# Kernel tuning notes

Hardware: AMD Instinct MI355X
Metric: run time of the kernel (lower is better)

The kernel has to match this reference:

```python
import jax, jax.numpy as jnp
import numpy as np

B, S, H, NH = 2, 2048, 1024, 16
D = H // NH

def setup_inputs() -> dict:
    key = jax.random.key(0)
    ks = jax.random.split(key, 9)
    s = 1.0 / np.sqrt(H)
    return {
        "x": jax.random.normal(ks[0], (B, S, H), jnp.float32),
        "wq": jax.random.uniform(ks[1], (H, H), jnp.float32, -s, s),
        "bq": jax.random.uniform(ks[2], (H,), jnp.float32, -s, s),
        "wk": jax.random.uniform(ks[3], (H, H), jnp.float32, -s, s),
        "bk": jax.random.uniform(ks[4], (H,), jnp.float32, -s, s),
        "wv": jax.random.uniform(ks[5], (H, H), jnp.float32, -s, s),
        "bv": jax.random.uniform(ks[6], (H,), jnp.float32, -s, s),
        "wo": jax.random.uniform(ks[7], (H, H), jnp.float32, -s, s),
        "bo": jax.random.uniform(ks[8], (H,), jnp.float32, -s, s),
    }

def _split_heads(t):
    # [B, S, H] -> [B, NH, S, D]
    return t.reshape(B, S, NH, D).transpose(0, 2, 1, 3)

def reference(x, wq, bq, wk, bk, wv, bv, wo, bo):
    q = _split_heads(x @ wq.T + bq)
    k = _split_heads(x @ wk.T + bk)
    v = _split_heads(x @ wv.T + bv)
    scores = jnp.einsum('bhqd,bhkd->bhqk', q, k) / jnp.sqrt(jnp.float32(D))
    attn = jax.nn.softmax(scores, axis=-1)  # full [B,NH,S,S] materialized as in source
    ctx = jnp.einsum('bhqk,bhkd->bhqd', attn, v)
    concat = ctx.transpose(0, 2, 1, 3).reshape(B, S, H)
    return concat @ wo.T + bo
```

## Files before the change

### kernel.cpp

```cpp
#include <hip/hip_runtime.h>
#include <cstdint>

typedef unsigned short u16;
typedef __attribute__((ext_vector_type(8))) short short8;
typedef __attribute__((ext_vector_type(4))) float f32x4;

#if __has_builtin(__builtin_amdgcn_exp2f)
#define EXP2F(x) __builtin_amdgcn_exp2f(x)
#else
#define EXP2F(x) exp2f(x)
#endif

__device__ inline u16 f2bf(float f) {
  union { float f; unsigned u; } v; v.f = f;
  unsigned u = v.u;
  return (u16)((u + 0x7fffu + ((u >> 16) & 1u)) >> 16);
}

__device__ inline unsigned pk2bf_fast(float a, float b) {
  union { float f; unsigned u; } ua, ub; ua.f = a; ub.f = b;
  return __builtin_amdgcn_perm(ub.u + 0x8000u, ua.u + 0x8000u, 0x07060302u);
}

__device__ inline void gl2lds16(const void* g, void* l) {
  __builtin_amdgcn_global_load_lds(
      (const __attribute__((address_space(1))) unsigned int*)(unsigned long long)(uintptr_t)g,
      (__attribute__((address_space(3))) unsigned int*)(unsigned int)(uintptr_t)l,
      16, 0, 0);
}


__global__ __launch_bounds__(256) void cvt_kernel(
    const float* __restrict__ x,
    const float* __restrict__ wq, const float* __restrict__ wk,
    const float* __restrict__ wv, const float* __restrict__ wo,
    u16* __restrict__ xb, u16* __restrict__ wqb, u16* __restrict__ wkb,
    u16* __restrict__ wvb, u16* __restrict__ wob) {
  const int y = blockIdx.y;
  const int Q = 1 << 20;
  const float* src;
  u16* dst;
  if (y < 4)       { src = x + y * Q; dst = xb + y * Q; }
  else if (y == 4) { src = wq; dst = wqb; }
  else if (y == 5) { src = wk; dst = wkb; }
  else if (y == 6) { src = wv; dst = wvb; }
  else             { src = wo; dst = wob; }
  const int i = (blockIdx.x * 256 + threadIdx.x) * 8;
  float4 a = *(const float4*)(src + i);
  float4 b = *(const float4*)(src + i + 4);
  short8 o;
  o[0] = (short)f2bf(a.x); o[1] = (short)f2bf(a.y);
  o[2] = (short)f2bf(a.z); o[3] = (short)f2bf(a.w);
  o[4] = (short)f2bf(b.x); o[5] = (short)f2bf(b.y);
  o[6] = (short)f2bf(b.z); o[7] = (short)f2bf(b.w);
  const int j = (i & ~63) | (((((i >> 3) & 7) ^ ((i >> 10) & 7))) << 3);
  *(short8*)(dst + j) = o;
}

__global__ __launch_bounds__(256) void gemm_qkv(
    const u16* __restrict__ xb,
    const u16* __restrict__ wqb, const u16* __restrict__ wkb, const u16* __restrict__ wvb,
    const float* __restrict__ bq, const float* __restrict__ bk, const float* __restrict__ bv,
    u16* __restrict__ qo, u16* __restrict__ ko, u16* __restrict__ vto) {
  const int z = blockIdx.z;
  const u16* W = (z == 0) ? wqb : (z == 1) ? wkb : wvb;
  const float* bias = (z == 0) ? bq : (z == 1) ? bk : bv;

  __shared__ u16 smem[32768];
  u16* As = smem;
  u16* Bs = smem + 16384;
  const int tid = threadIdx.x, lane = tid & 63;
  const int wid = tid >> 6, wm = wid >> 1, wn = wid & 1;
  const int l15 = lane & 15, lg = lane >> 4;
  const int m0 = blockIdx.y * 128, n0 = blockIdx.x * 128;
  const int sw = ((l15 & 7) << 3);

  f32x4 acc[4][4] = {};

#pragma unroll
  for (int i = 0; i < 4; ++i) {
    int c = i * 256 + tid;
    gl2lds16(xb + (m0 + (c >> 3)) * 1024 + (c & 7) * 8, As + c * 8);
    gl2lds16(W  + (n0 + (c >> 3)) * 1024 + (c & 7) * 8, Bs + c * 8);
  }

  for (int k0 = 0; k0 < 1024; k0 += 64) {
    const int p = (k0 >> 6) & 1;
    __syncthreads();
    if (k0 < 960) {
      u16* An = As + (1 - p) * 8192;
      u16* Bn = Bs + (1 - p) * 8192;
#pragma unroll
      for (int i = 0; i < 4; ++i) {
        int c = i * 256 + tid;
        gl2lds16(xb + (m0 + (c >> 3)) * 1024 + k0 + 64 + (c & 7) * 8, An + c * 8);
        gl2lds16(W  + (n0 + (c >> 3)) * 1024 + k0 + 64 + (c & 7) * 8, Bn + c * 8);
      }
    }
    const u16* Ap = As + p * 8192;
    const u16* Bp = Bs + p * 8192;
#pragma unroll
    for (int kk = 0; kk < 2; ++kk) {
      short8 af[4], bf[4];
#pragma unroll
      for (int mb = 0; mb < 4; ++mb)
        af[mb] = *(const short8*)(Ap + (wm * 64 + mb * 16 + l15) * 64 + ((((kk * 4 + lg) << 3) ^ sw)));
#pragma unroll
      for (int nb = 0; nb < 4; ++nb)
        bf[nb] = *(const short8*)(Bp + (wn * 64 + nb * 16 + l15) * 64 + ((((kk * 4 + lg) << 3) ^ sw)));
#pragma unroll
      for (int mb = 0; mb < 4; ++mb)
#pragma unroll
        for (int nb = 0; nb < 4; ++nb)
          acc[mb][nb] = __builtin_amdgcn_mfma_f32_16x16x32_bf16(af[mb], bf[nb], acc[mb][nb], 0, 0, 0);
    }
  }

  if (z < 2) {
    u16* out = (z == 0) ? qo : ko;
#pragma unroll
    for (int mb = 0; mb < 4; ++mb)
#pragma unroll
      for (int nb = 0; nb < 4; ++nb)
#pragma unroll
        for (int r = 0; r < 4; ++r) {
          int m = m0 + wm * 64 + mb * 16 + lg * 4 + r;
          int n = n0 + wn * 64 + nb * 16 + l15;
          float v = acc[mb][nb][r] + bias[n];
          int b = m >> 11, s = m & 2047, hh = n >> 6, d = n & 63;
          int dcol = (z == 0) ? d : ((((d >> 3) ^ (s & 7)) << 3) | (d & 7));
          out[((b * 16 + hh) * 2048 + s) * 64 + dcol] = f2bf(v);
        }
  } else {
    __syncthreads();
    u16* wbuf = smem + wid * 4608;
#pragma unroll
    for (int mb = 0; mb < 4; ++mb)
#pragma unroll
      for (int nb = 0; nb < 4; ++nb) {
        int n = n0 + wn * 64 + nb * 16 + l15;
        float bn = bias[n];
        int dl = nb * 16 + l15;
#pragma unroll
        for (int r = 0; r < 4; ++r) {
          int sig = (lg * 4 + r) * 4 + mb;
          wbuf[dl * 72 + sig] = f2bf(acc[mb][nb][r] + bn);
        }
      }
    int h_w = (n0 >> 6) + wn;
    int mbase = m0 + wm * 64;
    int b = mbase >> 11, sb = mbase & 2047;
#pragma unroll
    for (int i = 0; i < 8; ++i) {
      int dl = (lane >> 3) + 8 * i;
      int c = lane & 7;
      short8 vv = *(const short8*)(wbuf + dl * 72 + c * 8);
      int cs = c ^ (dl & 7);
      *(short8*)(vto + ((b * 16 + h_w) * 64 + dl) * 2048 + sb + cs * 8) = vv;
    }
  }
}

__global__ __launch_bounds__(256, 2) void attn_kernel(
    const u16* __restrict__ qg, const u16* __restrict__ kg,
    const u16* __restrict__ vtg, u16* __restrict__ ctxg) {
  const int h = blockIdx.x, qt = blockIdx.y, b = blockIdx.z;
  const int bh = b * 16 + h;
  const u16* Qg = qg + (bh * 2048 + qt * 128) * 64;
  const u16* Kg = kg + bh * 2048 * 64;
  const u16* Vg = vtg + bh * 64 * 2048;

  __shared__ u16 SP[128 * 72];
  __shared__ u16 KV[2][8192];

  const int tid = threadIdx.x, lane = tid & 63, wid = tid >> 6;
  const int l15 = lane & 15, lg = lane >> 4;
  const int row0 = wid * 32;
  const int sw = ((l15 & 7) << 3);

  short8 qf[2][2];
#pragma unroll
  for (int mb = 0; mb < 2; ++mb)
#pragma unroll
    for (int kk = 0; kk < 2; ++kk)
      qf[mb][kk] = *(const short8*)(Qg + (row0 + mb * 16 + l15) * 64 + kk * 32 + lg * 8);

  short8 ones8;
#pragma unroll
  for (int j = 0; j < 8; ++j) ones8[j] = (short)0x3F80;

#pragma unroll
  for (int i = 0; i < 2; ++i) {
    int c = i * 256 + tid;
    gl2lds16(Kg + c * 8, &KV[0][c * 8]);
    gl2lds16(Vg + (c >> 3) * 2048 + (c & 7) * 8, &KV[0][4096 + c * 8]);
  }

  f32x4 acc[2][5] = {};
  const float cexp = 0.18033688011112042f;

  for (int kt = 0; kt < 32; ++kt) {
    const int p = kt & 1;
    __syncthreads();
    if (kt < 31) {
#pragma unroll
      for (int i = 0; i < 2; ++i) {
        int c = i * 256 + tid;
        gl2lds16(Kg + (kt + 1) * 4096 + c * 8, &KV[1 - p][c * 8]);
        gl2lds16(Vg + (c >> 3) * 2048 + (kt + 1) * 64 + (c & 7) * 8, &KV[1 - p][4096 + c * 8]);
      }
    }
    const u16* Ks = &KV[p][0];
    const u16* Vts = &KV[p][4096];

    f32x4 sc[2][4] = {};
#pragma unroll
    for (int kk = 0; kk < 2; ++kk) {
      short8 bfr[4];
#pragma unroll
      for (int nb = 0; nb < 4; ++nb)
        bfr[nb] = *(const short8*)(Ks + (nb * 16 + l15) * 64 + ((((kk * 4 + lg) << 3)) ^ sw));
#pragma unroll
      for (int mb = 0; mb < 2; ++mb)
#pragma unroll
        for (int nb = 0; nb < 4; ++nb)
          sc[mb][nb] = __builtin_amdgcn_mfma_f32_16x16x32_bf16(qf[mb][kk], bfr[nb], sc[mb][nb], 0, 0, 0);
    }

#pragma unroll
    for (int mb = 0; mb < 2; ++mb)
#pragma unroll
      for (int r = 0; r < 4; ++r) {
        float p0 = EXP2F(fmaf(sc[mb][0][r], cexp, -4.0f));
        float p1 = EXP2F(fmaf(sc[mb][1][r], cexp, -4.0f));
        float p2 = EXP2F(fmaf(sc[mb][2][r], cexp, -4.0f));
        float p3 = EXP2F(fmaf(sc[mb][3][r], cexp, -4.0f));
        uint2 u;
        u.x = pk2bf_fast(p0, p1);
        u.y = pk2bf_fast(p2, p3);
        *(uint2*)(SP + (row0 + mb * 16 + lg * 4 + r) * 72 + l15 * 4) = u;
      }

#pragma unroll
    for (int kk = 0; kk < 2; ++kk) {
      short8 pa[2], vb[4];
#pragma unroll
      for (int mb = 0; mb < 2; ++mb)
        pa[mb] = *(const short8*)(SP + (row0 + mb * 16 + l15) * 72 + kk * 32 + lg * 8);
#pragma unroll
      for (int nd = 0; nd < 4; ++nd)
        vb[nd] = *(const short8*)(Vts + (nd * 16 + l15) * 64 + ((((kk * 4 + lg) << 3)) ^ sw));
#pragma unroll
      for (int mb = 0; mb < 2; ++mb) {
#pragma unroll
        for (int nd = 0; nd < 4; ++nd)
          acc[mb][nd] = __builtin_amdgcn_mfma_f32_16x16x32_bf16(pa[mb], vb[nd], acc[mb][nd], 0, 0, 0);
        acc[mb][4] = __builtin_amdgcn_mfma_f32_16x16x32_bf16(pa[mb], ones8, acc[mb][4], 0, 0, 0);
      }
    }
  }

#pragma unroll
  for (int mb = 0; mb < 2; ++mb)
#pragma unroll
    for (int r = 0; r < 4; ++r) {
      float inv = 1.0f / acc[mb][4][r];
      int s = qt * 128 + row0 + mb * 16 + lg * 4 + r;
      int s7 = s & 7;
      u16* dst = ctxg + (b * 2048 + s) * 1024 + h * 64;
#pragma unroll
      for (int nd = 0; nd < 4; ++nd) {
        int d = nd * 16 + l15;
        int dcol = (((d >> 3) ^ s7) << 3) | (d & 7);
        dst[dcol] = f2bf(acc[mb][nd][r] * inv);
      }
    }
}

__global__ __launch_bounds__(256) void gemm_out(
    const u16* __restrict__ cb, const u16* __restrict__ wob,
    const float* __restrict__ bo, float* __restrict__ out) {
  __shared__ u16 smem[24576];
  u16* As = smem;
  u16* Bs = smem + 16384;
  const int tid = threadIdx.x, lane = tid & 63;
  const int wid = tid >> 6;
  const int l15 = lane & 15, lg = lane >> 4;
  const int m0 = blockIdx.y * 128, n0 = blockIdx.x * 64;
  const int sw = ((l15 & 7) << 3);

  f32x4 acc[2][4] = {};

#pragma unroll
  for (int i = 0; i < 4; ++i) {
    int c = i * 256 + tid;
    gl2lds16(cb + (m0 + (c >> 3)) * 1024 + (c & 7) * 8, As + c * 8);
  }
#pragma unroll
  for (int i = 0; i < 2; ++i) {
    int c = i * 256 + tid;
    gl2lds16(wob + (n0 + (c >> 3)) * 1024 + (c & 7) * 8, Bs + c * 8);
  }

  for (int k0 = 0; k0 < 1024; k0 += 64) {
    const int p = (k0 >> 6) & 1;
    __syncthreads();
    if (k0 < 960) {
      u16* An = As + (1 - p) * 8192;
      u16* Bn = Bs + (1 - p) * 4096;
#pragma unroll
      for (int i = 0; i < 4; ++i) {
        int c = i * 256 + tid;
        gl2lds16(cb + (m0 + (c >> 3)) * 1024 + k0 + 64 + (c & 7) * 8, An + c * 8);
      }
#pragma unroll
      for (int i = 0; i < 2; ++i) {
        int c = i * 256 + tid;
        gl2lds16(wob + (n0 + (c >> 3)) * 1024 + k0 + 64 + (c & 7) * 8, Bn + c * 8);
      }
    }
    const u16* Ap = As + p * 8192;
    const u16* Bp = Bs + p * 4096;
#pragma unroll
    for (int kk = 0; kk < 2; ++kk) {
      short8 af[2], bf[4];
#pragma unroll
      for (int mb = 0; mb < 2; ++mb)
        af[mb] = *(const short8*)(Ap + (wid * 32 + mb * 16 + l15) * 64 + ((((kk * 4 + lg) << 3)) ^ sw));
#pragma unroll
      for (int nb = 0; nb < 4; ++nb)
        bf[nb] = *(const short8*)(Bp + (nb * 16 + l15) * 64 + ((((kk * 4 + lg) << 3)) ^ sw));
#pragma unroll
      for (int mb = 0; mb < 2; ++mb)
#pragma unroll
        for (int nb = 0; nb < 4; ++nb)
          acc[mb][nb] = __builtin_amdgcn_mfma_f32_16x16x32_bf16(af[mb], bf[nb], acc[mb][nb], 0, 0, 0);
    }
  }

#pragma unroll
  for (int mb = 0; mb < 2; ++mb)
#pragma unroll
    for (int nb = 0; nb < 4; ++nb)
#pragma unroll
      for (int r = 0; r < 4; ++r) {
        int m = m0 + wid * 32 + mb * 16 + lg * 4 + r;
        int n = n0 + nb * 16 + l15;
        out[m * 1024 + n] = acc[mb][nb][r] + bo[n];
      }
}

extern "C" void kernel_launch(void* const* d_in, const int* in_sizes, int n_in,
                              void* d_out, int out_size, void* d_ws, size_t ws_size,
                              hipStream_t stream) {
  const float* x  = (const float*)d_in[0];
  const float* wq = (const float*)d_in[1];
  const float* bq = (const float*)d_in[2];
  const float* wk = (const float*)d_in[3];
  const float* bk = (const float*)d_in[4];
  const float* wv = (const float*)d_in[5];
  const float* bv = (const float*)d_in[6];
  const float* wo = (const float*)d_in[7];
  const float* bo = (const float*)d_in[8];

  if (ws_size < (size_t)24 * 1024 * 1024 * 2) return;
  u16* xb   = (u16*)d_ws;
  u16* wqb  = xb  + (4u << 20);
  u16* wkb  = wqb + (1u << 20);
  u16* wvb  = wkb + (1u << 20);
  u16* wob  = wvb + (1u << 20);
  u16* qb   = wob + (1u << 20);
  u16* kb   = qb  + (4u << 20);
  u16* vtb  = kb  + (4u << 20);
  u16* ctxb = vtb + (4u << 20);

  cvt_kernel<<<dim3(512, 8, 1), 256, 0, stream>>>(x, wq, wk, wv, wo, xb, wqb, wkb, wvb, wob);
  gemm_qkv<<<dim3(8, 32, 3), 256, 0, stream>>>(xb, wqb, wkb, wvb, bq, bk, bv, qb, kb, vtb);
  attn_kernel<<<dim3(16, 16, 2), 256, 0, stream>>>(qb, kb, vtb, ctxb);
  gemm_out<<<dim3(16, 32, 1), 256, 0, stream>>>(ctxb, wob, bo, (float*)d_out);
}
```

Before: 190.0 us.

## Retile QKV, attention and output GEMM kernels for more blocks and per-wave reuse

The QKV GEMM tile shrinks from 128x128 to 128x64, doubling the grid, and the V-transpose epilogue is reworked into a shared staging buffer plus a cooperative store. The attention kernel drops to 128 threads with each wave owning 64 query rows, which raises K/V fragment reuse per LDS load but doubles register pressure. The output GEMM shrinks to 64x64 tiles to raise block count. Together these trade per-block reuse against occupancy and grid fill across the three kernels.

```diff
diff --git a/kernel.cpp b/kernel.cpp
--- a/kernel.cpp
+++ b/kernel.cpp
@@ -66,22 +66,26 @@
   const u16* W = (z == 0) ? wqb : (z == 1) ? wkb : wvb;
   const float* bias = (z == 0) ? bq : (z == 1) ? bk : bv;
 
-  __shared__ u16 smem[32768];
+  __shared__ u16 smem[24576];
   u16* As = smem;
   u16* Bs = smem + 16384;
   const int tid = threadIdx.x, lane = tid & 63;
-  const int wid = tid >> 6, wm = wid >> 1, wn = wid & 1;
+  const int wid = tid >> 6;
   const int l15 = lane & 15, lg = lane >> 4;
-  const int m0 = blockIdx.y * 128, n0 = blockIdx.x * 128;
+  const int m0 = blockIdx.y * 128, n0 = blockIdx.x * 64;
   const int sw = ((l15 & 7) << 3);
 
-  f32x4 acc[4][4] = {};
+  f32x4 acc[2][4] = {};
 
 #pragma unroll
   for (int i = 0; i < 4; ++i) {
     int c = i * 256 + tid;
     gl2lds16(xb + (m0 + (c >> 3)) * 1024 + (c & 7) * 8, As + c * 8);
-    gl2lds16(W  + (n0 + (c >> 3)) * 1024 + (c & 7) * 8, Bs + c * 8);
+  }
+#pragma unroll
+  for (int i = 0; i < 2; ++i) {
+    int c = i * 256 + tid;
+    gl2lds16(W + (n0 + (c >> 3)) * 1024 + (c & 7) * 8, Bs + c * 8);
   }
 
   for (int k0 = 0; k0 < 1024; k0 += 64) {
@@ -89,27 +93,31 @@
     __syncthreads();
     if (k0 < 960) {
       u16* An = As + (1 - p) * 8192;
-      u16* Bn = Bs + (1 - p) * 8192;
+      u16* Bn = Bs + (1 - p) * 4096;
 #pragma unroll
       for (int i = 0; i < 4; ++i) {
         int c = i * 256 + tid;
         gl2lds16(xb + (m0 + (c >> 3)) * 1024 + k0 + 64 + (c & 7) * 8, An + c * 8);
-        gl2lds16(W  + (n0 + (c >> 3)) * 1024 + k0 + 64 + (c & 7) * 8, Bn + c * 8);
+      }
+#pragma unroll
+      for (int i = 0; i < 2; ++i) {
+        int c = i * 256 + tid;
+        gl2lds16(W + (n0 + (c >> 3)) * 1024 + k0 + 64 + (c & 7) * 8, Bn + c * 8);
       }
     }
     const u16* Ap = As + p * 8192;
-    const u16* Bp = Bs + p * 8192;
+    const u16* Bp = Bs + p * 4096;
 #pragma unroll
     for (int kk = 0; kk < 2; ++kk) {
-      short8 af[4], bf[4];
-#pragma unroll
-      for (int mb = 0; mb < 4; ++mb)
-        af[mb] = *(const short8*)(Ap + (wm * 64 + mb * 16 + l15) * 64 + ((((kk * 4 + lg) << 3) ^ sw)));
-#pragma unroll
-      for (int nb = 0; nb < 4; ++nb)
-        bf[nb] = *(const short8*)(Bp + (wn * 64 + nb * 16 + l15) * 64 + ((((kk * 4 + lg) << 3) ^ sw)));
-#pragma unroll
-      for (int mb = 0; mb < 4; ++mb)
+      short8 af[2], bf[4];
+#pragma unroll
+      for (int mb = 0; mb < 2; ++mb)
+        af[mb] = *(const short8*)(Ap + (wid * 32 + mb * 16 + l15) * 64 + ((((kk * 4 + lg) << 3)) ^ sw));
+#pragma unroll
+      for (int nb = 0; nb < 4; ++nb)
+        bf[nb] = *(const short8*)(Bp + (nb * 16 + l15) * 64 + ((((kk * 4 + lg) << 3)) ^ sw));
+#pragma unroll
+      for (int mb = 0; mb < 2; ++mb)
 #pragma unroll
         for (int nb = 0; nb < 4; ++nb)
           acc[mb][nb] = __builtin_amdgcn_mfma_f32_16x16x32_bf16(af[mb], bf[nb], acc[mb][nb], 0, 0, 0);
@@ -119,13 +127,13 @@
   if (z < 2) {
     u16* out = (z == 0) ? qo : ko;
 #pragma unroll
-    for (int mb = 0; mb < 4; ++mb)
+    for (int mb = 0; mb < 2; ++mb)
 #pragma unroll
       for (int nb = 0; nb < 4; ++nb)
 #pragma unroll
         for (int r = 0; r < 4; ++r) {
-          int m = m0 + wm * 64 + mb * 16 + lg * 4 + r;
-          int n = n0 + wn * 64 + nb * 16 + l15;
+          int m = m0 + wid * 32 + mb * 16 + lg * 4 + r;
+          int n = n0 + nb * 16 + l15;
           float v = acc[mb][nb][r] + bias[n];
           int b = m >> 11, s = m & 2047, hh = n >> 6, d = n & 63;
           int dcol = (z == 0) ? d : ((((d >> 3) ^ (s & 7)) << 3) | (d & 7));
@@ -133,35 +141,38 @@
         }
   } else {
     __syncthreads();
-    u16* wbuf = smem + wid * 4608;
-#pragma unroll
-    for (int mb = 0; mb < 4; ++mb)
+    u16* wbuf = smem + (wid >> 1) * 4608;
+    const int so = (wid & 1) * 2;
+#pragma unroll
+    for (int mb = 0; mb < 2; ++mb)
 #pragma unroll
       for (int nb = 0; nb < 4; ++nb) {
-        int n = n0 + wn * 64 + nb * 16 + l15;
+        int n = n0 + nb * 16 + l15;
         float bn = bias[n];
         int dl = nb * 16 + l15;
 #pragma unroll
         for (int r = 0; r < 4; ++r) {
-          int sig = (lg * 4 + r) * 4 + mb;
+          int sig = (lg * 4 + r) * 4 + so + mb;
           wbuf[dl * 72 + sig] = f2bf(acc[mb][nb][r] + bn);
         }
       }
-    int h_w = (n0 >> 6) + wn;
-    int mbase = m0 + wm * 64;
-    int b = mbase >> 11, sb = mbase & 2047;
-#pragma unroll
-    for (int i = 0; i < 8; ++i) {
-      int dl = (lane >> 3) + 8 * i;
-      int c = lane & 7;
-      short8 vv = *(const short8*)(wbuf + dl * 72 + c * 8);
+    __syncthreads();
+    int hh = n0 >> 6;
+    int bb = m0 >> 11;
+    int sbase = m0 & 2047;
+#pragma unroll
+    for (int i = 0; i < 4; ++i) {
+      int idx = i * 256 + tid;
+      int p2 = idx >> 9, rem = idx & 511;
+      int dl = rem >> 3, c = rem & 7;
+      short8 vv = *(const short8*)(smem + p2 * 4608 + dl * 72 + c * 8);
       int cs = c ^ (dl & 7);
-      *(short8*)(vto + ((b * 16 + h_w) * 64 + dl) * 2048 + sb + cs * 8) = vv;
-    }
-  }
-}
-
-__global__ __launch_bounds__(256, 2) void attn_kernel(
+      *(short8*)(vto + ((bb * 16 + hh) * 64 + dl) * 2048 + sbase + p2 * 64 + cs * 8) = vv;
+    }
+  }
+}
+
+__global__ __launch_bounds__(128, 2) void attn_kernel(
     const u16* __restrict__ qg, const u16* __restrict__ kg,
     const u16* __restrict__ vtg, u16* __restrict__ ctxg) {
   const int h = blockIdx.x, qt = blockIdx.y, b = blockIdx.z;
@@ -175,12 +186,12 @@
 
   const int tid = threadIdx.x, lane = tid & 63, wid = tid >> 6;
   const int l15 = lane & 15, lg = lane >> 4;
-  const int row0 = wid * 32;
+  const int row0 = wid * 64;
   const int sw = ((l15 & 7) << 3);
 
-  short8 qf[2][2];
-#pragma unroll
-  for (int mb = 0; mb < 2; ++mb)
+  short8 qf[4][2];
+#pragma unroll
+  for (int mb = 0; mb < 4; ++mb)
 #pragma unroll
     for (int kk = 0; kk < 2; ++kk)
       qf[mb][kk] = *(const short8*)(Qg + (row0 + mb * 16 + l15) * 64 + kk * 32 + lg * 8);
@@ -190,13 +201,13 @@
   for (int j = 0; j < 8; ++j) ones8[j] = (short)0x3F80;
 
 #pragma unroll
-  for (int i = 0; i < 2; ++i) {
-    int c = i * 256 + tid;
+  for (int i = 0; i < 4; ++i) {
+    int c = i * 128 + tid;
     gl2lds16(Kg + c * 8, &KV[0][c * 8]);
     gl2lds16(Vg + (c >> 3) * 2048 + (c & 7) * 8, &KV[0][4096 + c * 8]);
   }
 
-  f32x4 acc[2][5] = {};
+  f32x4 acc[4][5] = {};
   const float cexp = 0.18033688011112042f;
 
   for (int kt = 0; kt < 32; ++kt) {
@@ -204,8 +215,8 @@
     __syncthreads();
     if (kt < 31) {
 #pragma unroll
-      for (int i = 0; i < 2; ++i) {
-        int c = i * 256 + tid;
+      for (int i = 0; i < 4; ++i) {
+        int c = i * 128 + tid;
         gl2lds16(Kg + (kt + 1) * 4096 + c * 8, &KV[1 - p][c * 8]);
         gl2lds16(Vg + (c >> 3) * 2048 + (kt + 1) * 64 + (c & 7) * 8, &KV[1 - p][4096 + c * 8]);
       }
@@ -213,7 +224,7 @@
     const u16* Ks = &KV[p][0];
     const u16* Vts = &KV[p][4096];
 
-    f32x4 sc[2][4] = {};
+    f32x4 sc[4][4] = {};
 #pragma unroll
     for (int kk = 0; kk < 2; ++kk) {
       short8 bfr[4];
@@ -221,14 +232,14 @@
       for (int nb = 0; nb < 4; ++nb)
         bfr[nb] = *(const short8*)(Ks + (nb * 16 + l15) * 64 + ((((kk * 4 + lg) << 3)) ^ sw));
 #pragma unroll
-      for (int mb = 0; mb < 2; ++mb)
+      for (int mb = 0; mb < 4; ++mb)
 #pragma unroll
         for (int nb = 0; nb < 4; ++nb)
           sc[mb][nb] = __builtin_amdgcn_mfma_f32_16x16x32_bf16(qf[mb][kk], bfr[nb], sc[mb][nb], 0, 0, 0);
     }
 
 #pragma unroll
-    for (int mb = 0; mb < 2; ++mb)
+    for (int mb = 0; mb < 4; ++mb)
 #pragma unroll
       for (int r = 0; r < 4; ++r) {
         float p0 = EXP2F(fmaf(sc[mb][0][r], cexp, -4.0f));
@@ -243,15 +254,15 @@
 
 #pragma unroll
     for (int kk = 0; kk < 2; ++kk) {
-      short8 pa[2], vb[4];
-#pragma unroll
-      for (int mb = 0; mb < 2; ++mb)
+      short8 pa[4], vb[4];
+#pragma unroll
+      for (int mb = 0; mb < 4; ++mb)
         pa[mb] = *(const short8*)(SP + (row0 + mb * 16 + l15) * 72 + kk * 32 + lg * 8);
 #pragma unroll
       for (int nd = 0; nd < 4; ++nd)
         vb[nd] = *(const short8*)(Vts + (nd * 16 + l15) * 64 + ((((kk * 4 + lg) << 3)) ^ sw));
 #pragma unroll
-      for (int mb = 0; mb < 2; ++mb) {
+      for (int mb = 0; mb < 4; ++mb) {
 #pragma unroll
         for (int nd = 0; nd < 4; ++nd)
           acc[mb][nd] = __builtin_amdgcn_mfma_f32_16x16x32_bf16(pa[mb], vb[nd], acc[mb][nd], 0, 0, 0);
@@ -261,7 +272,7 @@
   }
 
 #pragma unroll
-  for (int mb = 0; mb < 2; ++mb)
+  for (int mb = 0; mb < 4; ++mb)
 #pragma unroll
     for (int r = 0; r < 4; ++r) {
       float inv = 1.0f / acc[mb][4][r];
@@ -280,25 +291,21 @@
 __global__ __launch_bounds__(256) void gemm_out(
     const u16* __restrict__ cb, const u16* __restrict__ wob,
     const float* __restrict__ bo, float* __restrict__ out) {
-  __shared__ u16 smem[24576];
+  __shared__ u16 smem[16384];
   u16* As = smem;
-  u16* Bs = smem + 16384;
+  u16* Bs = smem + 8192;
   const int tid = threadIdx.x, lane = tid & 63;
   const int wid = tid >> 6;
   const int l15 = lane & 15, lg = lane >> 4;
-  const int m0 = blockIdx.y * 128, n0 = blockIdx.x * 64;
+  const int m0 = blockIdx.y * 64, n0 = blockIdx.x * 64;
   const int sw = ((l15 & 7) << 3);
 
-  f32x4 acc[2][4] = {};
-
-#pragma unroll
-  for (int i = 0; i < 4; ++i) {
-    int c = i * 256 + tid;
-    gl2lds16(cb + (m0 + (c >> 3)) * 1024 + (c & 7) * 8, As + c * 8);
-  }
+  f32x4 acc[4] = {};
+
 #pragma unroll
   for (int i = 0; i < 2; ++i) {
     int c = i * 256 + tid;
+    gl2lds16(cb  + (m0 + (c >> 3)) * 1024 + (c & 7) * 8, As + c * 8);
     gl2lds16(wob + (n0 + (c >> 3)) * 1024 + (c & 7) * 8, Bs + c * 8);
   }
 
@@ -306,48 +313,38 @@
     const int p = (k0 >> 6) & 1;
     __syncthreads();
     if (k0 < 960) {
-      u16* An = As + (1 - p) * 8192;
+      u16* An = As + (1 - p) * 4096;
       u16* Bn = Bs + (1 - p) * 4096;
-#pragma unroll
-      for (int i = 0; i < 4; ++i) {
-        int c = i * 256 + tid;
-        gl2lds16(cb + (m0 + (c >> 3)) * 1024 + k0 + 64 + (c & 7) * 8, An + c * 8);
-      }
 #pragma unroll
       for (int i = 0; i < 2; ++i) {
         int c = i * 256 + tid;
+        gl2lds16(cb  + (m0 + (c >> 3)) * 1024 + k0 + 64 + (c & 7) * 8, An + c * 8);
         gl2lds16(wob + (n0 + (c >> 3)) * 1024 + k0 + 64 + (c & 7) * 8, Bn + c * 8);
       }
     }
-    const u16* Ap = As + p * 8192;
+    const u16* Ap = As + p * 4096;
     const u16* Bp = Bs + p * 4096;
 #pragma unroll
     for (int kk = 0; kk < 2; ++kk) {
-      short8 af[2], bf[4];
-#pragma unroll
-      for (int mb = 0; mb < 2; ++mb)
-        af[mb] = *(const short8*)(Ap + (wid * 32 + mb * 16 + l15) * 64 + ((((kk * 4 + lg) << 3)) ^ sw));
+      short8 af, bf[4];
+      af = *(const short8*)(Ap + (wid * 16 + l15) * 64 + ((((kk * 4 + lg) << 3)) ^ sw));
 #pragma unroll
       for (int nb = 0; nb < 4; ++nb)
         bf[nb] = *(const short8*)(Bp + (nb * 16 + l15) * 64 + ((((kk * 4 + lg) << 3)) ^ sw));
 #pragma unroll
-      for (int mb = 0; mb < 2; ++mb)
-#pragma unroll
-        for (int nb = 0; nb < 4; ++nb)
-          acc[mb][nb] = __builtin_amdgcn_mfma_f32_16x16x32_bf16(af[mb], bf[nb], acc[mb][nb], 0, 0, 0);
-    }
-  }
-
-#pragma unroll
-  for (int mb = 0; mb < 2; ++mb)
-#pragma unroll
-    for (int nb = 0; nb < 4; ++nb)
-#pragma unroll
-      for (int r = 0; r < 4; ++r) {
-        int m = m0 + wid * 32 + mb * 16 + lg * 4 + r;
-        int n = n0 + nb * 16 + l15;
-        out[m * 1024 + n] = acc[mb][nb][r] + bo[n];
-      }
+      for (int nb = 0; nb < 4; ++nb)
+        acc[nb] = __builtin_amdgcn_mfma_f32_16x16x32_bf16(af, bf[nb], acc[nb], 0, 0, 0);
+    }
+  }
+
+#pragma unroll
+  for (int nb = 0; nb < 4; ++nb)
+#pragma unroll
+    for (int r = 0; r < 4; ++r) {
+      int m = m0 + wid * 16 + lg * 4 + r;
+      int n = n0 + nb * 16 + l15;
+      out[m * 1024 + n] = acc[nb][r] + bo[n];
+    }
 }
 
 extern "C" void kernel_launch(void* const* d_in, const int* in_sizes, int n_in,
@@ -375,7 +372,7 @@
   u16* ctxb = vtb + (4u << 20);
 
   cvt_kernel<<<dim3(512, 8, 1), 256, 0, stream>>>(x, wq, wk, wv, wo, xb, wqb, wkb, wvb, wob);
-  gemm_qkv<<<dim3(8, 32, 3), 256, 0, stream>>>(xb, wqb, wkb, wvb, bq, bk, bv, qb, kb, vtb);
-  attn_kernel<<<dim3(16, 16, 2), 256, 0, stream>>>(qb, kb, vtb, ctxb);
-  gemm_out<<<dim3(16, 32, 1), 256, 0, stream>>>(ctxb, wob, bo, (float*)d_out);
-}
+  gemm_qkv<<<dim3(16, 32, 3), 256, 0, stream>>>(xb, wqb, wkb, wvb, bq, bk, bv, qb, kb, vtb);
+  attn_kernel<<<dim3(16, 16, 2), 128, 0, stream>>>(qb, kb, vtb, ctxb);
+  gemm_out<<<dim3(16, 64, 1), 256, 0, stream>>>(ctxb, wob, bo, (float*)d_out);
+}
```

Result: slower. 216.6 us (+14.0%).
